# Kernel optimization log

Measured on AMD Instinct MI355X. Metric: run time of the kernel, lower is better.

## Reference

```python
import jax, jax.numpy as jnp
import numpy as np
import math

B, L, CH, H, NL, N2 = 32, 4096, 1, 256, 4, 32  # batch, seq, channels, d_model, n_layers, d_state//2
LN_EPS = 1e-5


def setup_inputs() -> dict:
    key = jax.random.key(0)
    ks = jax.random.split(key, 12)
    rn = lambda k, shape, s=1.0: (jax.random.normal(k, shape, dtype=jnp.float32) * s)
    inp = {}
    inp["x"] = rn(ks[0], (B, L, CH))
    inp["enc_w"] = rn(ks[1], (H, CH), 1.0 / math.sqrt(CH))
    inp["enc_b"] = jnp.zeros((H,), jnp.float32)
    # S4D kernel parameters, stacked over layers (standard S4D init)
    dt_min, dt_max = 1e-3, 1e-1
    u = jax.random.uniform(ks[2], (NL, H))
    inp["log_dt"] = (u * (math.log(dt_max) - math.log(dt_min)) + math.log(dt_min)).astype(jnp.float32)
    inp["log_A_real"] = jnp.full((NL, H, N2), math.log(0.5), jnp.float32)
    inp["A_imag"] = jnp.broadcast_to(math.pi * jnp.arange(N2, dtype=jnp.float32), (NL, H, N2)) + jnp.zeros((NL, H, N2), jnp.float32)
    inp["C_re"] = rn(ks[3], (NL, H, N2))
    inp["C_im"] = rn(ks[4], (NL, H, N2))
    inp["D"] = rn(ks[5], (NL, H))
    # output_linear: 1x1 Conv1d H->2H followed by GLU
    inp["glu_w"] = rn(ks[6], (NL, 2 * H, H), 1.0 / math.sqrt(H))
    inp["glu_b"] = jnp.zeros((NL, 2 * H), jnp.float32)
    inp["ln_g"] = jnp.ones((NL, H), jnp.float32)
    inp["ln_b"] = jnp.zeros((NL, H), jnp.float32)
    inp["dec1_w"] = rn(ks[7], (1, L), 1.0 / math.sqrt(L))
    inp["dec1_b"] = jnp.zeros((1,), jnp.float32)
    inp["dec2_w"] = rn(ks[8], (1, H), 1.0 / math.sqrt(H))
    inp["dec2_b"] = jnp.zeros((1,), jnp.float32)
    return inp


def _s4d_layer(u_bhl, log_dt, log_A_real, A_imag, C_re, C_im, D, glu_w, glu_b):
    """S4D block on (B, H, L): FFT conv with diagonal-SSM kernel + skip D + GELU + GLU output linear."""
    Lx = u_bhl.shape[-1]
    dt = jnp.exp(log_dt)                          # (H,)
    A = -jnp.exp(log_A_real) + 1j * A_imag        # (H, N2) complex
    C = C_re + 1j * C_im                          # (H, N2)
    dtA = A * dt[:, None]                         # (H, N2)
    Ck = C * (jnp.exp(dtA) - 1.0) / A             # ZOH-style discretized C
    # Vandermonde kernel: k[h, l] = 2 * Re( sum_n Ck[h,n] * exp(dtA[h,n] * l) )
    expdtA = jnp.exp(dtA[:, :, None] * jnp.arange(Lx, dtype=jnp.float32))  # (H, N2, L)
    k = 2.0 * jnp.einsum('hn,hnl->hl', Ck, expdtA).real                    # (H, L)
    # causal conv via zero-padded FFT
    kf = jnp.fft.rfft(k, n=2 * Lx)
    uf = jnp.fft.rfft(u_bhl, n=2 * Lx)
    y = jnp.fft.irfft(uf * kf, n=2 * Lx)[..., :Lx]
    y = y + u_bhl * D[:, None]
    y = jax.nn.gelu(y, approximate=False)
    # 1x1 conv H -> 2H, then GLU over the channel dim
    y = jnp.einsum('oh,bhl->bol', glu_w, y) + glu_b[:, None]
    a, g = jnp.split(y, 2, axis=-2)
    return a * jax.nn.sigmoid(g)


def reference(x, enc_w, enc_b, log_dt, log_A_real, A_imag, C_re, C_im, D,
              glu_w, glu_b, ln_g, ln_b, dec1_w, dec1_b, dec2_w, dec2_b):
    h = x @ enc_w.T + enc_b                 # (B, L, H)
    h = jnp.swapaxes(h, -1, -2)             # (B, H, L)
    for i in range(NL):
        z = _s4d_layer(h, log_dt[i], log_A_real[i], A_imag[i], C_re[i], C_im[i],
                       D[i], glu_w[i], glu_b[i])
        h = z + h                           # residual (dropout = identity in eval)
        ht = jnp.swapaxes(h, -1, -2)        # (B, L, H) -> LayerNorm over H (postnorm)
        mu = ht.mean(-1, keepdims=True)
        var = ht.var(-1, keepdims=True)
        ht = (ht - mu) / jnp.sqrt(var + LN_EPS) * ln_g[i] + ln_b[i]
        h = jnp.swapaxes(ht, -1, -2)
    y = jnp.einsum('bhl,ol->bho', h, dec1_w) + dec1_b   # (B, H, 1)
    y = y.squeeze(-1)                                    # (B, H)
    y = y @ dec2_w.T + dec2_b                            # (B, 1)
    y = y.squeeze(-1)                                    # (B,)
    return jax.nn.sigmoid(y)
```

## Files before the change

### kernel.cpp

```cpp
#include <hip/hip_runtime.h>
#include <math.h>

#define WS_WT   16777216
#define WS_Y1   17039360
#define WS_A256 17047552
#define WS_V    17063936
#define WS_ABUF 19161088
#define WS_S    29646848

typedef unsigned short ushort_t;
struct __attribute__((aligned(8))) us4 { ushort_t x, y, z, w; };
typedef short bf16x8 __attribute__((ext_vector_type(8)));
typedef float f32x4  __attribute__((ext_vector_type(4)));

__device__ __forceinline__ float bf2f(ushort_t u) {
    union { unsigned int i; float f; } c; c.i = ((unsigned int)u) << 16; return c.f;
}
__device__ __forceinline__ ushort_t f2bf(float f) {
    union { float f; unsigned int i; } c; c.f = f;
    unsigned int x = c.i;
    unsigned int r = (x + 0x7FFF + ((x >> 16) & 1)) >> 16;
    return (ushort_t)r;
}
__device__ __forceinline__ float fast_gelu(float v) {
    float y = 1.5957691216057308f * (v + 0.044715f * v * v * v);
    return v / (1.f + __expf(-y));
}

__global__ __launch_bounds__(256) void enc_kernel(const float* __restrict__ x,
    const float* __restrict__ ew, const float* __restrict__ eb, ushort_t* __restrict__ Hb)
{
    int i = blockIdx.x * 256 + threadIdx.x;
    int l8 = i & 511;
    int h  = (i >> 9) & 255;
    int b  = i >> 17;
    const float* xp = x + ((size_t)b << 12) + (l8 << 3);
    float4 a0 = ((const float4*)xp)[0];
    float4 a1 = ((const float4*)xp)[1];
    float w = ew[h], bb = eb[h];
    us4 o0, o1;
    o0.x = f2bf(fmaf(a0.x, w, bb)); o0.y = f2bf(fmaf(a0.y, w, bb));
    o0.z = f2bf(fmaf(a0.z, w, bb)); o0.w = f2bf(fmaf(a0.w, w, bb));
    o1.x = f2bf(fmaf(a1.x, w, bb)); o1.y = f2bf(fmaf(a1.y, w, bb));
    o1.z = f2bf(fmaf(a1.z, w, bb)); o1.w = f2bf(fmaf(a1.w, w, bb));
    us4* op = (us4*)(Hb + ((size_t)i << 3));
    op[0] = o0; op[1] = o1;
}

__global__ __launch_bounds__(256) void wtb_kernel(const float* __restrict__ gw, ushort_t* __restrict__ wTb)
{
    int i = blockIdx.x * 256 + threadIdx.x;
    wTb[i] = f2bf(gw[i]);
}

__global__ __launch_bounds__(256) void prep_kernel(
    const float* __restrict__ log_dt, const float* __restrict__ lAr,
    const float* __restrict__ Aim_, const float* __restrict__ Cre,
    const float* __restrict__ Cim, ushort_t* __restrict__ Abuf,
    ushort_t* __restrict__ Vg, float* __restrict__ a256tab, int li)
{
    __shared__ float s_ar[32], s_ai[32], s_ckr[32], s_cki[32];
    __shared__ float powr[8][32], powi[8][32];
    __shared__ float karr[256];
    __shared__ ushort_t Vt[256][66];
    int t = threadIdx.x;
    int h = blockIdx.x;
    int pb = (li * 256 + h) * 32;

    if (t < 32) {
        int s = t;
        float dt = expf(log_dt[li * 256 + h]);
        float Are = -expf(lAr[pb + s]);
        float Ai  = Aim_[pb + s];
        float e = expf(Are * dt);
        float ar = e * cosf(Ai * dt), ai = e * sinf(Ai * dt);
        float inv = 1.f / (Are * Are + Ai * Ai);
        float numr = ar - 1.f, numi = ai;
        float tr = (numr * Are + numi * Ai) * inv;
        float ti = (numi * Are - numr * Ai) * inv;
        float cr = Cre[pb + s], ci = Cim[pb + s];
        s_ar[s] = ar; s_ai[s] = ai;
        s_ckr[s] = 2.f * (cr * tr - ci * ti);
        s_cki[s] = 2.f * (cr * ti + ci * tr);
        float xr = ar, xi = ai;
        for (int k = 0; k < 8; k++) {
            powr[k][s] = xr; powi[k][s] = xi;
            float nr = xr * xr - xi * xi;
            float ni = 2.f * xr * xi;
            xr = nr; xi = ni;
        }
        a256tab[h * 64 + s * 2] = xr;
        a256tab[h * 64 + s * 2 + 1] = xi;
    }
    __syncthreads();

    int d = t;
    float adr[32], adi[32];
    #pragma unroll
    for (int s = 0; s < 32; s++) { adr[s] = 1.f; adi[s] = 0.f; }
    #pragma unroll
    for (int bit = 0; bit < 8; bit++) {
        if (d & (1 << bit)) {
            #pragma unroll
            for (int s = 0; s < 32; s++) {
                float pr_ = powr[bit][s], pi_ = powi[bit][s];
                float nr = adr[s] * pr_ - adi[s] * pi_;
                float ni = adr[s] * pi_ + adi[s] * pr_;
                adr[s] = nr; adi[s] = ni;
            }
        }
    }
    float kd = 0.f;
    #pragma unroll
    for (int s = 0; s < 32; s++) kd += s_ckr[s] * adr[s] - s_cki[s] * adi[s];
    karr[d] = kd;
    unsigned int wrow[32];
    #pragma unroll
    for (int s = 0; s < 32; s++) {
        float wr = adr[s] * s_ar[s] - adi[s] * s_ai[s];
        float wi = adr[s] * s_ai[s] + adi[s] * s_ar[s];
        float v0 = s_ckr[s] * wr - s_cki[s] * wi;
        float v1 = -(s_ckr[s] * wi + s_cki[s] * wr);
        wrow[s] = (unsigned int)f2bf(v0) | ((unsigned int)f2bf(v1) << 16);
    }
    {
        ushort_t* arow = Abuf + (size_t)h * 81920 + (size_t)d * 320 + 256;
        #pragma unroll
        for (int q = 0; q < 8; q++) {
            uint4 v; v.x = wrow[q*4]; v.y = wrow[q*4+1]; v.z = wrow[q*4+2]; v.w = wrow[q*4+3];
            *(uint4*)(arow + q * 8) = v;
        }
    }
    {
        int e = 255 - d;
        float evr[32], evi[32];
        #pragma unroll
        for (int s = 0; s < 32; s++) { evr[s] = 1.f; evi[s] = 0.f; }
        #pragma unroll
        for (int bit = 0; bit < 8; bit++) {
            if (e & (1 << bit)) {
                #pragma unroll
                for (int s = 0; s < 32; s++) {
                    float pr_ = powr[bit][s], pi_ = powi[bit][s];
                    float nr = evr[s] * pr_ - evi[s] * pi_;
                    float ni = evr[s] * pi_ + evi[s] * pr_;
                    evr[s] = nr; evi[s] = ni;
                }
            }
        }
        #pragma unroll
        for (int s = 0; s < 32; s++) {
            Vt[d][2*s]   = f2bf(evr[s]);
            Vt[d][2*s+1] = f2bf(evi[s]);
        }
    }
    __syncthreads();

    {
        ushort_t* trow = Abuf + (size_t)h * 81920 + (size_t)t * 320;
        for (int j4 = 0; j4 < 64; j4++) {
            int j = j4 * 4;
            us4 v;
            v.x = (j     <= t) ? f2bf(karr[t - j    ]) : (ushort_t)0;
            v.y = (j + 1 <= t) ? f2bf(karr[t - j - 1]) : (ushort_t)0;
            v.z = (j + 2 <= t) ? f2bf(karr[t - j - 2]) : (ushort_t)0;
            v.w = (j + 3 <= t) ? f2bf(karr[t - j - 3]) : (ushort_t)0;
            *(us4*)(trow + j) = v;
        }
    }
    {
        int m = t >> 2, jq = t & 3;
        ushort_t* vrow = Vg + (size_t)h * 16384 + (size_t)m * 256 + jq * 64;
        for (int j4 = 0; j4 < 16; j4++) {
            int j = jq * 64 + j4 * 4;
            us4 v;
            v.x = Vt[j][m]; v.y = Vt[j+1][m]; v.z = Vt[j+2][m]; v.w = Vt[j+3][m];
            *(us4*)(vrow + j4 * 4) = v;
        }
    }
}

__global__ __launch_bounds__(256, 2) void vgemm_kernel(
    const ushort_t* __restrict__ U, const ushort_t* __restrict__ Vg,
    ushort_t* __restrict__ Sb, int b0, int ntot)
{
    __shared__ ushort_t yt[64 * 256];
    int t = threadIdx.x;
    int h = blockIdx.x;
    int tile = blockIdx.y;
    int nl = t & 63, kq = t >> 6;
    int n = tile * 64 + nl;
    const ushort_t* ub = U + (size_t)(b0 + (n >> 4)) * 1048576 + (size_t)h * 4096 + (n & 15) * 256;
    #pragma unroll
    for (int i = 0; i < 8; i++) {
        int c = kq * 8 + i;
        *(uint4*)(&yt[nl * 256 + ((c ^ (nl & 7)) << 3)]) = *(const uint4*)(ub + c * 8);
    }
    __syncthreads();

    int lane = t & 63, w = t >> 6;
    int ln15 = lane & 15, quad = lane >> 4;
    const ushort_t* va = Vg + (size_t)h * 16384 + (size_t)(w * 16 + ln15) * 256;
    f32x4 acc[4] = {};
    for (int ks = 0; ks < 8; ks++) {
        int c = ks * 4 + quad;
        bf16x8 af = *(const bf16x8*)(va + ks * 32 + quad * 8);
        #pragma unroll
        for (int nt = 0; nt < 4; nt++) {
            bf16x8 bf_ = *(const bf16x8*)(&yt[(nt * 16 + ln15) * 256 + ((c ^ (ln15 & 7)) << 3)]);
            acc[nt] = __builtin_amdgcn_mfma_f32_16x16x32_bf16(af, bf_, acc[nt], 0, 0, 0);
        }
    }
    #pragma unroll
    for (int nt = 0; nt < 4; nt++) {
        int nn = tile * 64 + nt * 16 + ln15;
        ushort_t* sp = Sb + ((size_t)h * ntot + nn) * 64 + w * 16 + quad * 4;
        us4 v;
        v.x = f2bf(acc[nt][0]); v.y = f2bf(acc[nt][1]);
        v.z = f2bf(acc[nt][2]); v.w = f2bf(acc[nt][3]);
        *(us4*)sp = v;
    }
}

__global__ __launch_bounds__(256) void scan_kernel(
    ushort_t* __restrict__ Sb, const float* __restrict__ a256tab, int ntot)
{
    int t = threadIdx.x;
    int lane = t & 63;
    int w = t >> 6;
    int sub = lane >> 5, s = lane & 31;
    int r = blockIdx.x * 8 + w * 2 + sub;
    int h = r & 255, bl = r >> 8;
    float m2r = a256tab[h * 64 + s * 2], m2i = a256tab[h * 64 + s * 2 + 1];
    float sr = 0.f, si = 0.f;
    for (int c = 0; c < 16; c++) {
        unsigned int* p = (unsigned int*)Sb + ((size_t)h * ntot + bl * 16 + c) * 32 + s;
        unsigned int sv = *p;
        float Sr = bf2f((ushort_t)(sv & 0xFFFF));
        float Si = bf2f((ushort_t)(sv >> 16));
        *p = (unsigned int)f2bf(sr) | ((unsigned int)f2bf(si) << 16);
        float nsr = m2r * sr - m2i * si + Sr;
        float nsi = m2r * si + m2i * sr + Si;
        sr = nsr; si = nsi;
    }
}

__global__ __launch_bounds__(256, 2) void dgemm_kernel(
    const ushort_t* __restrict__ U, const ushort_t* __restrict__ Abuf,
    const ushort_t* __restrict__ Sb, const float* __restrict__ Dp,
    ushort_t* __restrict__ G, int li, int b0, int ntot)
{
    __shared__ ushort_t yt[64 * 320];
    int t = threadIdx.x;
    int h = blockIdx.x;
    int tile = blockIdx.y;
    int nl = t & 63, kq = t >> 6;
    int n = tile * 64 + nl;
    int sw = nl & 7;
    const ushort_t* ub = U + (size_t)(b0 + (n >> 4)) * 1048576 + (size_t)h * 4096 + (n & 15) * 256;
    #pragma unroll
    for (int i = 0; i < 8; i++) {
        int c = kq * 8 + i;
        *(uint4*)(&yt[nl * 320 + ((c ^ sw) << 3)]) = *(const uint4*)(ub + c * 8);
    }
    {
        const uint4* sp = (const uint4*)(Sb + ((size_t)h * ntot + n) * 64 + kq * 16);
        int c0 = 32 + kq * 2;
        *(uint4*)(&yt[nl * 320 + ((c0 ^ sw) << 3)]) = sp[0];
        *(uint4*)(&yt[nl * 320 + (((c0 + 1) ^ sw) << 3)]) = sp[1];
    }
    __syncthreads();

    int lane = t & 63, w = t >> 6;
    int ln15 = lane & 15, quad = lane >> 4;
    int rsw = ln15 & 7;
    const ushort_t* Ah = Abuf + (size_t)h * 81920;
    f32x4 acc[4][4] = {};
    for (int ks = 0; ks < 10; ks++) {
        int kk = ks * 32 + quad * 8;
        int c = ks * 4 + quad;
        bf16x8 af[4];
        #pragma unroll
        for (int mt = 0; mt < 4; mt++)
            af[mt] = *(const bf16x8*)(Ah + (size_t)(w * 64 + mt * 16 + ln15) * 320 + kk);
        #pragma unroll
        for (int nt = 0; nt < 4; nt++) {
            bf16x8 bf_ = *(const bf16x8*)(&yt[(nt * 16 + ln15) * 320 + ((c ^ rsw) << 3)]);
            #pragma unroll
            for (int mt = 0; mt < 4; mt++)
                acc[mt][nt] = __builtin_amdgcn_mfma_f32_16x16x32_bf16(af[mt], bf_, acc[mt][nt], 0, 0, 0);
        }
    }
    float Dh = Dp[li * 256 + h];
    #pragma unroll
    for (int mt = 0; mt < 4; mt++) {
        #pragma unroll
        for (int nt = 0; nt < 4; nt++) {
            int nn = tile * 64 + nt * 16 + ln15;
            int lb = w * 64 + mt * 16 + quad * 4;
            int c = lb >> 3, co = lb & 7;
            us4 uv = *(const us4*)(&yt[(nt * 16 + ln15) * 320 + ((c ^ rsw) << 3) + co]);
            float uu[4] = {bf2f(uv.x), bf2f(uv.y), bf2f(uv.z), bf2f(uv.w)};
            us4 o;
            ushort_t* op = &o.x;
            #pragma unroll
            for (int rr = 0; rr < 4; rr++) {
                float v = acc[mt][nt][rr] + Dh * uu[rr];
                op[rr] = f2bf(fast_gelu(v));
            }
            ushort_t* gp = G + ((size_t)(nn >> 4) * 256 + h) * 4096 + (nn & 15) * 256 + lb;
            *(us4*)gp = o;
        }
    }
}

#define LDK 268
__global__ __launch_bounds__(256, 2) void gluln_kernel(
    const ushort_t* __restrict__ G, const ushort_t* __restrict__ wTb,
    const float* __restrict__ glu_b, const float* __restrict__ ln_g,
    const float* __restrict__ ln_b, ushort_t* __restrict__ Hb, int li, int b0)
{
    __shared__ ushort_t yt[64 * LDK];
    __shared__ float sred[4][64], sqred[4][64];
    __shared__ float mup[64], rstd[64];
    int t = threadIdx.x;
    int pf = blockIdx.x * 64;
    int bloc = pf >> 12;
    int l0 = pf & 4095;
    int b = b0 + bloc;

    const ushort_t* gb = G + (size_t)bloc * 1048576 + l0;
    unsigned int* dst = (unsigned int*)&yt[0];
    #pragma unroll
    for (int i = 0; i < 4; i++) {
        int hp = ((i & 1) << 6) + (t >> 2);
        int pg = ((i >> 1) << 2) + (t & 3);
        int h0 = hp * 2;
        uint4 va = *(const uint4*)(gb + (size_t)h0 * 4096 + pg * 8);
        uint4 vb = *(const uint4*)(gb + (size_t)(h0 + 1) * 4096 + pg * 8);
        const ushort_t* ra = (const ushort_t*)&va;
        const ushort_t* rb = (const ushort_t*)&vb;
        #pragma unroll
        for (int j = 0; j < 8; j++) {
            unsigned int v = (unsigned int)ra[j] | ((unsigned int)rb[j] << 16);
            dst[(pg * 8 + j) * (LDK / 2) + hp] = v;
        }
    }
    __syncthreads();

    int lane = t & 63, w = t >> 6;
    int ln15 = lane & 15, quad = lane >> 4;
    int oA = w * 64;
    const ushort_t* wA = wTb + li * 131072;

    f32x4 accA[4][4] = {};
    f32x4 accG[4][4] = {};

    for (int ks = 0; ks < 8; ks++) {
        int kk = ks * 32 + quad * 8;
        bf16x8 af[4], gf[4];
        #pragma unroll
        for (int mt = 0; mt < 4; mt++) {
            int oa = oA + mt * 16 + ln15;
            af[mt] = *(const bf16x8*)(wA + (size_t)oa * 256 + kk);
            gf[mt] = *(const bf16x8*)(wA + (size_t)(oa + 256) * 256 + kk);
        }
        bf16x8 bfr[4];
        #pragma unroll
        for (int nt = 0; nt < 4; nt++) {
            const us4* yp = (const us4*)&yt[(nt * 16 + ln15) * LDK + kk];
            us4 lo = yp[0], hi = yp[1];
            bf16x8 v;
            v[0] = (short)lo.x; v[1] = (short)lo.y; v[2] = (short)lo.z; v[3] = (short)lo.w;
            v[4] = (short)hi.x; v[5] = (short)hi.y; v[6] = (short)hi.z; v[7] = (short)hi.w;
            bfr[nt] = v;
        }
        #pragma unroll
        for (int mt = 0; mt < 4; mt++)
            #pragma unroll
            for (int nt = 0; nt < 4; nt++) {
                accA[mt][nt] = __builtin_amdgcn_mfma_f32_16x16x32_bf16(bfr[nt], af[mt], accA[mt][nt], 0, 0, 0);
                accG[mt][nt] = __builtin_amdgcn_mfma_f32_16x16x32_bf16(bfr[nt], gf[mt], accG[mt][nt], 0, 0, 0);
            }
    }

    ushort_t* hb_ = Hb + (size_t)b * 1048576;
    us4 hold[4][4];
    #pragma unroll
    for (int mt = 0; mt < 4; mt++) {
        const ushort_t* hrow = hb_ + (size_t)(oA + mt * 16 + ln15) * 4096 + l0 + quad * 4;
        #pragma unroll
        for (int nt = 0; nt < 4; nt++)
            hold[mt][nt] = *(const us4*)(hrow + nt * 16);
    }

    float ba[4], bg[4];
    #pragma unroll
    for (int mt = 0; mt < 4; mt++) {
        int o = oA + mt * 16 + ln15;
        ba[mt] = glu_b[li * 512 + o];
        bg[mt] = glu_b[li * 512 + 256 + o];
    }

    float psl[4][4] = {}, pql[4][4] = {};
    #pragma unroll
    for (int mt = 0; mt < 4; mt++) {
        #pragma unroll
        for (int nt = 0; nt < 4; nt++) {
            const ushort_t* hp4 = &hold[mt][nt].x;
            #pragma unroll
            for (int r = 0; r < 4; r++) {
                float a = accA[mt][nt][r] + ba[mt];
                float g = accG[mt][nt][r] + bg[mt];
                float z = a / (1.f + __expf(-g));
                float hn = z + bf2f(hp4[r]);
                accA[mt][nt][r] = hn;
                psl[nt][r] += hn; pql[nt][r] = fmaf(hn, hn, pql[nt][r]);
            }
        }
    }
    #pragma unroll
    for (int nt = 0; nt < 4; nt++)
        #pragma unroll
        for (int r = 0; r < 4; r++) {
            float s = psl[nt][r], q = pql[nt][r];
            s += __shfl_xor(s, 1, 64); q += __shfl_xor(q, 1, 64);
            s += __shfl_xor(s, 2, 64); q += __shfl_xor(q, 2, 64);
            s += __shfl_xor(s, 4, 64); q += __shfl_xor(q, 4, 64);
            s += __shfl_xor(s, 8, 64); q += __shfl_xor(q, 8, 64);
            psl[nt][r] = s; pql[nt][r] = q;
        }
    if (ln15 == 0) {
        #pragma unroll
        for (int nt = 0; nt < 4; nt++)
            #pragma unroll
            for (int r = 0; r < 4; r++) {
                int p = nt * 16 + quad * 4 + r;
                sred[w][p] = psl[nt][r];
                sqred[w][p] = pql[nt][r];
            }
    }
    __syncthreads();
    if (t < 64) {
        float S = (sred[0][t] + sred[1][t]) + (sred[2][t] + sred[3][t]);
        float Q = (sqred[0][t] + sqred[1][t]) + (sqred[2][t] + sqred[3][t]);
        float mu = S * (1.f / 256.f);
        float var = Q * (1.f / 256.f) - mu * mu;
        mup[t] = mu; rstd[t] = rsqrtf(var + 1e-5f);
    }
    __syncthreads();

    #pragma unroll
    for (int mt = 0; mt < 4; mt++) {
        int o = oA + mt * 16 + ln15;
        float gm = ln_g[li * 256 + o];
        float bt = ln_b[li * 256 + o];
        ushort_t* hrow = hb_ + (size_t)o * 4096 + l0 + quad * 4;
        #pragma unroll
        for (int nt = 0; nt < 4; nt++) {
            us4 ov;
            ushort_t* op = &ov.x;
            #pragma unroll
            for (int r = 0; r < 4; r++) {
                int p = nt * 16 + quad * 4 + r;
                float v = (accA[mt][nt][r] - mup[p]) * rstd[p] * gm + bt;
                op[r] = f2bf(v);
            }
            *(us4*)(hrow + nt * 16) = ov;
        }
    }
}

__global__ __launch_bounds__(256) void dec1_kernel(const ushort_t* __restrict__ Hb,
    const float* __restrict__ w1, const float* __restrict__ b1, float* __restrict__ y1)
{
    int bh = blockIdx.x;
    const ushort_t* base = Hb + (size_t)bh * 4096;
    int t = threadIdx.x;
    float s = 0.f;
    for (int l = t; l < 4096; l += 256) s = fmaf(bf2f(base[l]), w1[l], s);
    #pragma unroll
    for (int d = 32; d > 0; d >>= 1) s += __shfl_xor(s, d, 64);
    __shared__ float red[4];
    if ((t & 63) == 0) red[t >> 6] = s;
    __syncthreads();
    if (t == 0) y1[bh] = red[0] + red[1] + red[2] + red[3] + b1[0];
}

__global__ __launch_bounds__(256) void dec2_kernel(const float* __restrict__ y1,
    const float* __restrict__ w2, const float* __restrict__ b2, float* __restrict__ out)
{
    int t = threadIdx.x;
    int b = blockIdx.x * 4 + (t >> 6);
    int lane = t & 63;
    float s = 0.f;
    #pragma unroll
    for (int k = 0; k < 4; k++) s = fmaf(y1[b * 256 + lane + k * 64], w2[lane + k * 64], s);
    #pragma unroll
    for (int d = 32; d > 0; d >>= 1) s += __shfl_xor(s, d, 64);
    if (lane == 0) out[b] = 1.f / (1.f + expf(-(s + b2[0])));
}

extern "C" void kernel_launch(void* const* d_in, const int* in_sizes, int n_in,
                              void* d_out, int out_size, void* d_ws, size_t ws_size,
                              hipStream_t stream)
{
    const float* x      = (const float*)d_in[0];
    const float* enc_w  = (const float*)d_in[1];
    const float* enc_b  = (const float*)d_in[2];
    const float* log_dt = (const float*)d_in[3];
    const float* lAr    = (const float*)d_in[4];
    const float* Aim    = (const float*)d_in[5];
    const float* Cre    = (const float*)d_in[6];
    const float* Cim    = (const float*)d_in[7];
    const float* Dp     = (const float*)d_in[8];
    const float* glu_w  = (const float*)d_in[9];
    const float* glu_b  = (const float*)d_in[10];
    const float* ln_g   = (const float*)d_in[11];
    const float* ln_b   = (const float*)d_in[12];
    const float* w1     = (const float*)d_in[13];
    const float* b1     = (const float*)d_in[14];
    const float* w2     = (const float*)d_in[15];
    const float* b2     = (const float*)d_in[16];

    float* ws = (float*)d_ws;
    ushort_t* Hb   = (ushort_t*)ws;
    ushort_t* wTb  = (ushort_t*)(ws + WS_WT);
    float* y1      = ws + WS_Y1;
    float* a256    = ws + WS_A256;
    ushort_t* Vg   = (ushort_t*)(ws + WS_V);
    ushort_t* Abuf = (ushort_t*)(ws + WS_ABUF);
    float* outp    = (float*)d_out;

    size_t wsf = ws_size / 4;
    int nb = 32;
    while (nb > 4 && (size_t)WS_S + (size_t)nb * 655360 > wsf) nb >>= 1;
    int ntot = nb * 16;
    ushort_t* Sb = (ushort_t*)(ws + WS_S);
    ushort_t* Gb = (ushort_t*)(ws + WS_S + (size_t)nb * 131072);

    wtb_kernel<<<2048, 256, 0, stream>>>(glu_w, wTb);
    enc_kernel<<<16384, 256, 0, stream>>>(x, enc_w, enc_b, Hb);
    for (int li = 0; li < 4; li++) {
        prep_kernel<<<256, 256, 0, stream>>>(log_dt, lAr, Aim, Cre, Cim, Abuf, Vg, a256, li);
        for (int b0 = 0; b0 < 32; b0 += nb) {
            vgemm_kernel<<<dim3(256, nb / 4), 256, 0, stream>>>(Hb, Vg, Sb, b0, ntot);
            scan_kernel<<<nb * 32, 256, 0, stream>>>(Sb, a256, ntot);
            dgemm_kernel<<<dim3(256, nb / 4), 256, 0, stream>>>(Hb, Abuf, Sb, Dp, Gb, li, b0, ntot);
            gluln_kernel<<<nb * 64, 256, 0, stream>>>(Gb, wTb, glu_b, ln_g, ln_b, Hb, li, b0);
        }
    }
    dec1_kernel<<<8192, 256, 0, stream>>>(Hb, w1, b1, y1);
    dec2_kernel<<<8, 256, 0, stream>>>(y1, w2, b2, outp);
}
```

Before: 1.162 ms.

## Fuse chunk-state GEMM, inter-chunk scan and output GEMM into one kernel

Merges vgemm, scan and dgemm into a single s4df kernel. Each block computes its chunk end-states with MFMA into shared memory, runs the 16-step complex scan for its 4 sequences in shared memory, and writes the scanned states straight into the B-operand tile. This removes two kernel launches per layer and the global round-trips through the state buffer Sb. The cost is extra shared memory, two more barriers, and a serial scan that uses only half the threads while the rest wait.

```diff
diff --git a/kernel.cpp b/kernel.cpp
--- a/kernel.cpp
+++ b/kernel.cpp
@@ -180,77 +180,13 @@
     }
 }
 
-__global__ __launch_bounds__(256, 2) void vgemm_kernel(
-    const ushort_t* __restrict__ U, const ushort_t* __restrict__ Vg,
-    ushort_t* __restrict__ Sb, int b0, int ntot)
-{
-    __shared__ ushort_t yt[64 * 256];
-    int t = threadIdx.x;
-    int h = blockIdx.x;
-    int tile = blockIdx.y;
-    int nl = t & 63, kq = t >> 6;
-    int n = tile * 64 + nl;
-    const ushort_t* ub = U + (size_t)(b0 + (n >> 4)) * 1048576 + (size_t)h * 4096 + (n & 15) * 256;
-    #pragma unroll
-    for (int i = 0; i < 8; i++) {
-        int c = kq * 8 + i;
-        *(uint4*)(&yt[nl * 256 + ((c ^ (nl & 7)) << 3)]) = *(const uint4*)(ub + c * 8);
-    }
-    __syncthreads();
-
-    int lane = t & 63, w = t >> 6;
-    int ln15 = lane & 15, quad = lane >> 4;
-    const ushort_t* va = Vg + (size_t)h * 16384 + (size_t)(w * 16 + ln15) * 256;
-    f32x4 acc[4] = {};
-    for (int ks = 0; ks < 8; ks++) {
-        int c = ks * 4 + quad;
-        bf16x8 af = *(const bf16x8*)(va + ks * 32 + quad * 8);
-        #pragma unroll
-        for (int nt = 0; nt < 4; nt++) {
-            bf16x8 bf_ = *(const bf16x8*)(&yt[(nt * 16 + ln15) * 256 + ((c ^ (ln15 & 7)) << 3)]);
-            acc[nt] = __builtin_amdgcn_mfma_f32_16x16x32_bf16(af, bf_, acc[nt], 0, 0, 0);
-        }
-    }
-    #pragma unroll
-    for (int nt = 0; nt < 4; nt++) {
-        int nn = tile * 64 + nt * 16 + ln15;
-        ushort_t* sp = Sb + ((size_t)h * ntot + nn) * 64 + w * 16 + quad * 4;
-        us4 v;
-        v.x = f2bf(acc[nt][0]); v.y = f2bf(acc[nt][1]);
-        v.z = f2bf(acc[nt][2]); v.w = f2bf(acc[nt][3]);
-        *(us4*)sp = v;
-    }
-}
-
-__global__ __launch_bounds__(256) void scan_kernel(
-    ushort_t* __restrict__ Sb, const float* __restrict__ a256tab, int ntot)
-{
-    int t = threadIdx.x;
-    int lane = t & 63;
-    int w = t >> 6;
-    int sub = lane >> 5, s = lane & 31;
-    int r = blockIdx.x * 8 + w * 2 + sub;
-    int h = r & 255, bl = r >> 8;
-    float m2r = a256tab[h * 64 + s * 2], m2i = a256tab[h * 64 + s * 2 + 1];
-    float sr = 0.f, si = 0.f;
-    for (int c = 0; c < 16; c++) {
-        unsigned int* p = (unsigned int*)Sb + ((size_t)h * ntot + bl * 16 + c) * 32 + s;
-        unsigned int sv = *p;
-        float Sr = bf2f((ushort_t)(sv & 0xFFFF));
-        float Si = bf2f((ushort_t)(sv >> 16));
-        *p = (unsigned int)f2bf(sr) | ((unsigned int)f2bf(si) << 16);
-        float nsr = m2r * sr - m2i * si + Sr;
-        float nsi = m2r * si + m2i * sr + Si;
-        sr = nsr; si = nsi;
-    }
-}
-
-__global__ __launch_bounds__(256, 2) void dgemm_kernel(
+__global__ __launch_bounds__(256, 2) void s4df_kernel(
     const ushort_t* __restrict__ U, const ushort_t* __restrict__ Abuf,
-    const ushort_t* __restrict__ Sb, const float* __restrict__ Dp,
-    ushort_t* __restrict__ G, int li, int b0, int ntot)
+    const ushort_t* __restrict__ Vg, const float* __restrict__ a256tab,
+    const float* __restrict__ Dp, ushort_t* __restrict__ G, int li, int b0)
 {
     __shared__ ushort_t yt[64 * 320];
+    __shared__ ushort_t sS[64 * 66];
     int t = threadIdx.x;
     int h = blockIdx.x;
     int tile = blockIdx.y;
@@ -263,17 +199,56 @@
         int c = kq * 8 + i;
         *(uint4*)(&yt[nl * 320 + ((c ^ sw) << 3)]) = *(const uint4*)(ub + c * 8);
     }
-    {
-        const uint4* sp = (const uint4*)(Sb + ((size_t)h * ntot + n) * 64 + kq * 16);
-        int c0 = 32 + kq * 2;
-        *(uint4*)(&yt[nl * 320 + ((c0 ^ sw) << 3)]) = sp[0];
-        *(uint4*)(&yt[nl * 320 + (((c0 + 1) ^ sw) << 3)]) = sp[1];
-    }
     __syncthreads();
 
     int lane = t & 63, w = t >> 6;
     int ln15 = lane & 15, quad = lane >> 4;
     int rsw = ln15 & 7;
+
+    {
+        const ushort_t* va = Vg + (size_t)h * 16384 + (size_t)(w * 16 + ln15) * 256;
+        f32x4 acc[4] = {};
+        for (int ks = 0; ks < 8; ks++) {
+            int c = ks * 4 + quad;
+            bf16x8 af = *(const bf16x8*)(va + ks * 32 + quad * 8);
+            #pragma unroll
+            for (int nt = 0; nt < 4; nt++) {
+                bf16x8 bf_ = *(const bf16x8*)(&yt[(nt * 16 + ln15) * 320 + ((c ^ rsw) << 3)]);
+                acc[nt] = __builtin_amdgcn_mfma_f32_16x16x32_bf16(af, bf_, acc[nt], 0, 0, 0);
+            }
+        }
+        #pragma unroll
+        for (int nt = 0; nt < 4; nt++) {
+            int m = w * 16 + quad * 4;
+            int nn = nt * 16 + ln15;
+            sS[(m    ) * 66 + nn] = f2bf(acc[nt][0]);
+            sS[(m + 1) * 66 + nn] = f2bf(acc[nt][1]);
+            sS[(m + 2) * 66 + nn] = f2bf(acc[nt][2]);
+            sS[(m + 3) * 66 + nn] = f2bf(acc[nt][3]);
+        }
+    }
+    __syncthreads();
+
+    if (t < 128) {
+        int bq = t >> 5, s = t & 31;
+        float m2r = a256tab[h * 64 + s * 2], m2i = a256tab[h * 64 + s * 2 + 1];
+        int col = 256 + 2 * s;
+        int cc = col >> 3, off = col & 7;
+        float sr = 0.f, si = 0.f;
+        for (int c = 0; c < 16; c++) {
+            int nn = bq * 16 + c;
+            float Sr = bf2f(sS[(2 * s) * 66 + nn]);
+            float Si = bf2f(sS[(2 * s + 1) * 66 + nn]);
+            int addr = nn * 320 + ((cc ^ (nn & 7)) << 3) + off;
+            yt[addr] = f2bf(sr);
+            yt[addr + 1] = f2bf(si);
+            float nsr = m2r * sr - m2i * si + Sr;
+            float nsi = m2r * si + m2i * sr + Si;
+            sr = nsr; si = nsi;
+        }
+    }
+    __syncthreads();
+
     const ushort_t* Ah = Abuf + (size_t)h * 81920;
     f32x4 acc[4][4] = {};
     for (int ks = 0; ks < 10; ks++) {
@@ -535,8 +510,6 @@
     size_t wsf = ws_size / 4;
     int nb = 32;
     while (nb > 4 && (size_t)WS_S + (size_t)nb * 655360 > wsf) nb >>= 1;
-    int ntot = nb * 16;
-    ushort_t* Sb = (ushort_t*)(ws + WS_S);
     ushort_t* Gb = (ushort_t*)(ws + WS_S + (size_t)nb * 131072);
 
     wtb_kernel<<<2048, 256, 0, stream>>>(glu_w, wTb);
@@ -544,9 +517,7 @@
     for (int li = 0; li < 4; li++) {
         prep_kernel<<<256, 256, 0, stream>>>(log_dt, lAr, Aim, Cre, Cim, Abuf, Vg, a256, li);
         for (int b0 = 0; b0 < 32; b0 += nb) {
-            vgemm_kernel<<<dim3(256, nb / 4), 256, 0, stream>>>(Hb, Vg, Sb, b0, ntot);
-            scan_kernel<<<nb * 32, 256, 0, stream>>>(Sb, a256, ntot);
-            dgemm_kernel<<<dim3(256, nb / 4), 256, 0, stream>>>(Hb, Abuf, Sb, Dp, Gb, li, b0, ntot);
+            s4df_kernel<<<dim3(256, nb / 4), 256, 0, stream>>>(Hb, Abuf, Vg, a256, Dp, Gb, li, b0);
             gluln_kernel<<<nb * 64, 256, 0, stream>>>(Gb, wTb, glu_b, ln_g, ln_b, Hb, li, b0);
         }
     }
```

Result: faster. 1.019 ms (-12.3%).
